# Performance work log

Measured on AMD Instinct MI355X. Metric: run time of the kernel, lower is better.

The kernel has to match this reference:

```python
import jax, jax.numpy as jnp
import numpy as np

DELTA_V = 0.5
DELTA_D = 1.5
ALPHA = 1.0
BETA = 1.0
GAMMA = 0.001
K = 33  # label ids 0..32; 0 = background (ignored)
EPS = 1e-12


def setup_inputs() -> dict:
    key = jax.random.key(0)
    k1, k2 = jax.random.split(key)
    B, N, E = 8, 65536, 32
    embeddings = jax.random.normal(k1, (B, N, E), dtype=jnp.float32)
    labels = jax.random.randint(k2, (B, N), 0, K)
    return {"embeddings": embeddings, "labels": labels}


def reference(embeddings, labels):
    B, N, E = embeddings.shape
    dt = embeddings.dtype
    seg = (labels + jnp.arange(B)[:, None] * K).reshape(-1)  # (B*N,)

    # segment mean -> per-instance centers (B, K, E)
    sums = jax.ops.segment_sum(embeddings.reshape(B * N, E), seg, num_segments=B * K).reshape(B, K, E)
    counts = jax.ops.segment_sum(jnp.ones((B * N,), dtype=dt), seg, num_segments=B * K).reshape(B, K)
    centers = sums / jnp.maximum(counts, 1.0)[..., None]

    present = counts > 0
    present = present.at[:, 0].set(False)  # drop background label 0
    presf = present.astype(dt)
    n_inst = presf.sum(axis=1)  # (B,)

    # ---- variance term: per-point hinge distance to own center, segment-mean ----
    c_per_point = centers[jnp.arange(B)[:, None], labels]  # (B, N, E) gather
    d2 = ((embeddings - c_per_point) ** 2).sum(-1)
    dist = jnp.sqrt(jnp.maximum(d2, EPS))
    hinge = jnp.where(labels > 0, jnp.maximum(dist - DELTA_V, 0.0), 0.0)
    per_inst_sum = jax.ops.segment_sum(hinge.reshape(-1), seg, num_segments=B * K).reshape(B, K)
    per_inst_mean = per_inst_sum / jnp.maximum(counts, 1.0)
    variance_term = (per_inst_mean * presf).sum(1) / jnp.maximum(n_inst, 1.0)

    # ---- distance term: pairwise hinge between present instance centers ----
    diff2 = ((centers[:, :, None, :] - centers[:, None, :, :]) ** 2).sum(-1)  # (B,K,K)
    upper = jnp.triu(jnp.ones((K, K), dtype=bool), 1)[None]
    pair_valid = present[:, :, None] & present[:, None, :] & upper
    cd = jnp.sqrt(jnp.maximum(jnp.where(pair_valid, diff2, 1.0), EPS))
    pair_hinge = jnp.maximum(2.0 * DELTA_D - cd, 0.0) * pair_valid.astype(dt)
    n_pairs = n_inst * (n_inst - 1.0) * 0.5
    distance_term = pair_hinge.sum((1, 2)) / jnp.maximum(n_pairs, 1.0)

    # ---- regularization: mean L2 norm of present centers ----
    c_norm = jnp.sqrt(jnp.maximum((centers ** 2).sum(-1), EPS))
    reg_term = (c_norm * presf).sum(1) / jnp.maximum(n_inst, 1.0)

    per_batch = ALPHA * variance_term + BETA * distance_term + GAMMA * reg_term
    per_batch = jnp.where(n_inst > 0, per_batch, 0.0)
    return per_batch.sum() / B
```

## Files before the change

### kernel.cpp

```cpp
#include <hip/hip_runtime.h>
#include <math.h>

#define KC 33
#define ED 32
#define KE (KC * ED)
#define PAD 33

#define BPB_A 64
#define TPA 128
#define NSLOT 8
#define BPB_H 128
#define TPH 256


__global__ void k_zero(float* __restrict__ ws, int n, float* __restrict__ out) {
    int i = blockIdx.x * blockDim.x + threadIdx.x;
    if (i < n) ws[i] = 0.f;
    if (i == 0) out[0] = 0.f;
}

__global__ __launch_bounds__(256) void k_accum(const float* __restrict__ emb,
                                               const int* __restrict__ lab,
                                               float* __restrict__ sums,
                                               float* __restrict__ counts, int N) {
    __shared__ float s_tile[TPA * PAD];
    __shared__ float s_priv[NSLOT * KE];
    __shared__ int   s_lab[TPA];
    __shared__ float s_hist[2 * KC];
    int t = threadIdx.x;
    for (int i = t; i < NSLOT * KE; i += 256) s_priv[i] = 0.f;
    if (t < 2 * KC) s_hist[t] = 0.f;

    int b     = blockIdx.x / BPB_A;
    int blk   = blockIdx.x % BPB_A;
    int chunk = N / BPB_A;
    int e     = t & 31;
    int slot  = t >> 5;
    size_t pbase = (size_t)b * N + (size_t)blk * chunk;
    const int NT = chunk / TPA;

    const float4* g4 = (const float4*)(emb + pbase * ED);
    float4 r0 = g4[t], r1 = g4[t + 256], r2 = g4[t + 512], r3 = g4[t + 768];
    int rl = 0;
    if (t < TPA) rl = lab[pbase + t];
    __syncthreads();

    for (int tb = 0; tb < NT; tb++) {
        {
            int f, p, m;
            f = t;        p = f >> 3; m = (f & 7) * 4;
            { float* d = &s_tile[PAD * p + m]; d[0]=r0.x; d[1]=r0.y; d[2]=r0.z; d[3]=r0.w; }
            f = t + 256;  p = f >> 3; m = (f & 7) * 4;
            { float* d = &s_tile[PAD * p + m]; d[0]=r1.x; d[1]=r1.y; d[2]=r1.z; d[3]=r1.w; }
            f = t + 512;  p = f >> 3; m = (f & 7) * 4;
            { float* d = &s_tile[PAD * p + m]; d[0]=r2.x; d[1]=r2.y; d[2]=r2.z; d[3]=r2.w; }
            f = t + 768;  p = f >> 3; m = (f & 7) * 4;
            { float* d = &s_tile[PAD * p + m]; d[0]=r3.x; d[1]=r3.y; d[2]=r3.z; d[3]=r3.w; }
        }
        if (t < TPA) {
            s_lab[t] = rl;
            atomicAdd(&s_hist[(t >> 6) * KC + rl], 1.f);
        }
        __syncthreads();

        if (tb + 1 < NT) {
            const float4* gn = (const float4*)(emb + (pbase + (size_t)(tb + 1) * TPA) * ED);
            r0 = gn[t]; r1 = gn[t + 256]; r2 = gn[t + 512]; r3 = gn[t + 768];
            if (t < TPA) rl = lab[pbase + (size_t)(tb + 1) * TPA + t];
        }

        float* priv = &s_priv[slot * KE];
#pragma unroll
        for (int st = 0; st < TPA / NSLOT; st++) {
            int pt = st * NSLOT + slot;
            float x = s_tile[pt * PAD + e];
            int   k = s_lab[pt];
            priv[k * ED + e] += x;
        }
        __syncthreads();
    }

    for (int i = t; i < KE; i += 256) {
        float v = 0.f;
#pragma unroll
        for (int s = 0; s < NSLOT; s++) v += s_priv[s * KE + i];
        atomicAdd(&sums[(size_t)b * KE + i], v);
    }
    if (t < KC)
        atomicAdd(&counts[b * KC + t], s_hist[t] + s_hist[KC + t]);
}

__global__ __launch_bounds__(256) void k_hinge(const float* __restrict__ emb,
                                               const int* __restrict__ lab,
                                               const float* __restrict__ sums,
                                               const float* __restrict__ counts,
                                               float* __restrict__ var, int N) {
    __shared__ float s_tile[TPH * PAD];
    __shared__ float s_ctr[KC * PAD];
    __shared__ float s_cnt[KC];
    __shared__ float s_inv[KC];
    __shared__ int   s_lab[TPH];
    __shared__ float s_red[4];
    int t     = threadIdx.x;
    int b     = blockIdx.x / BPB_H;
    int blk   = blockIdx.x % BPB_H;
    int chunk = N / BPB_H;
    size_t pbase = (size_t)b * N + (size_t)blk * chunk;
    const int NT = chunk / TPH;

    const float4* g4 = (const float4*)(emb + pbase * ED);
    float4 r0 = g4[t],        r1 = g4[t + 256],  r2 = g4[t + 512],  r3 = g4[t + 768];
    float4 r4 = g4[t + 1024], r5 = g4[t + 1280], r6 = g4[t + 1536], r7 = g4[t + 1792];
    int rl = lab[pbase + t];

    if (t < KC) {
        float c = counts[b * KC + t];
        s_cnt[t] = fmaxf(c, 1.f);
        s_inv[t] = (t > 0 && c > 0.f) ? 1.f / fmaxf(c, 1.f) : 0.f;
    }
    __syncthreads();
    for (int i = t; i < KE; i += 256) {
        int k = i >> 5, e = i & 31;
        s_ctr[k * PAD + e] = sums[(size_t)b * KE + i] / s_cnt[k];
    }

    float hs = 0.f;
    for (int tb = 0; tb < NT; tb++) {
        {
            int f, p, m;
            f = t;         p = f >> 3; m = (f & 7) * 4;
            { float* d = &s_tile[PAD * p + m]; d[0]=r0.x; d[1]=r0.y; d[2]=r0.z; d[3]=r0.w; }
            f = t + 256;   p = f >> 3; m = (f & 7) * 4;
            { float* d = &s_tile[PAD * p + m]; d[0]=r1.x; d[1]=r1.y; d[2]=r1.z; d[3]=r1.w; }
            f = t + 512;   p = f >> 3; m = (f & 7) * 4;
            { float* d = &s_tile[PAD * p + m]; d[0]=r2.x; d[1]=r2.y; d[2]=r2.z; d[3]=r2.w; }
            f = t + 768;   p = f >> 3; m = (f & 7) * 4;
            { float* d = &s_tile[PAD * p + m]; d[0]=r3.x; d[1]=r3.y; d[2]=r3.z; d[3]=r3.w; }
            f = t + 1024;  p = f >> 3; m = (f & 7) * 4;
            { float* d = &s_tile[PAD * p + m]; d[0]=r4.x; d[1]=r4.y; d[2]=r4.z; d[3]=r4.w; }
            f = t + 1280;  p = f >> 3; m = (f & 7) * 4;
            { float* d = &s_tile[PAD * p + m]; d[0]=r5.x; d[1]=r5.y; d[2]=r5.z; d[3]=r5.w; }
            f = t + 1536;  p = f >> 3; m = (f & 7) * 4;
            { float* d = &s_tile[PAD * p + m]; d[0]=r6.x; d[1]=r6.y; d[2]=r6.z; d[3]=r6.w; }
            f = t + 1792;  p = f >> 3; m = (f & 7) * 4;
            { float* d = &s_tile[PAD * p + m]; d[0]=r7.x; d[1]=r7.y; d[2]=r7.z; d[3]=r7.w; }
        }
        s_lab[t] = rl;
        __syncthreads();

        if (tb + 1 < NT) {
            const float4* gn = (const float4*)(emb + (pbase + (size_t)(tb + 1) * TPH) * ED);
            r0 = gn[t];        r1 = gn[t + 256];  r2 = gn[t + 512];  r3 = gn[t + 768];
            r4 = gn[t + 1024]; r5 = gn[t + 1280]; r6 = gn[t + 1536]; r7 = gn[t + 1792];
            rl = lab[pbase + (size_t)(tb + 1) * TPH + t];
        }

        int   k  = s_lab[t];
        float iv = s_inv[k];
        const float* xr = &s_tile[t * PAD];
        const float* cr = &s_ctr[k * PAD];
        float d2 = 0.f;
#pragma unroll
        for (int j = 0; j < ED; j++) {
            float d = xr[j] - cr[j];
            d2 = fmaf(d, d, d2);
        }
        float dist = sqrtf(fmaxf(d2, 1e-12f));
        hs += fmaxf(dist - 0.5f, 0.f) * iv;
        __syncthreads();
    }

    hs += __shfl_xor(hs, 1);  hs += __shfl_xor(hs, 2);  hs += __shfl_xor(hs, 4);
    hs += __shfl_xor(hs, 8);  hs += __shfl_xor(hs, 16); hs += __shfl_xor(hs, 32);
    if ((t & 63) == 0) s_red[t >> 6] = hs;
    __syncthreads();
    if (t == 0)
        atomicAdd(&var[b], s_red[0] + s_red[1] + s_red[2] + s_red[3]);
}

__global__ __launch_bounds__(256) void k_final(const float* __restrict__ sums,
                                               const float* __restrict__ counts,
                                               const float* __restrict__ var,
                                               float* __restrict__ out, int B) {
    __shared__ float s_ctr[KE];
    __shared__ float s_cnt[KC];
    __shared__ float s_reg[KC];
    __shared__ int   s_prs[KC];
    __shared__ float s_red[256];
    int b = blockIdx.x;
    int t = threadIdx.x;

    if (t < KC) {
        float c = counts[b * KC + t];
        s_cnt[t] = fmaxf(c, 1.f);
        s_prs[t] = (t > 0 && c > 0.f) ? 1 : 0;
    }
    __syncthreads();
    for (int i = t; i < KE; i += 256)
        s_ctr[i] = sums[(size_t)b * KE + i] / s_cnt[i >> 5];
    __syncthreads();
    if (t < KC) {
        float n2 = 0.f;
        for (int e2 = 0; e2 < ED; e2++) { float c = s_ctr[t * ED + e2]; n2 += c * c; }
        s_reg[t] = s_prs[t] ? sqrtf(fmaxf(n2, 1e-12f)) : 0.f;
    }
    __syncthreads();

    float psum = 0.f;
    for (int q = t; q < KC * KC; q += 256) {
        int i = q / KC, j = q % KC;
        if (i < j && s_prs[i] && s_prs[j]) {
            float d2 = 0.f;
            for (int e2 = 0; e2 < ED; e2++) {
                float d = s_ctr[i * ED + e2] - s_ctr[j * ED + e2];
                d2 += d * d;
            }
            float cd = sqrtf(fmaxf(d2, 1e-12f));
            psum += fmaxf(3.0f - cd, 0.f);
        }
    }
    s_red[t] = psum;
    __syncthreads();
    for (int s = 128; s > 0; s >>= 1) {
        if (t < s) s_red[t] += s_red[t + s];
        __syncthreads();
    }

    if (t == 0) {
        float reg = 0.f; int n = 0;
        for (int k = 0; k < KC; k++) { reg += s_reg[k]; n += s_prs[k]; }
        float nf = (float)n;
        float variance_term = var[b] / fmaxf(nf, 1.f);
        float npairs = nf * (nf - 1.f) * 0.5f;
        float distance_term = s_red[0] / fmaxf(npairs, 1.f);
        float reg_term = reg / fmaxf(nf, 1.f);
        float pb = variance_term + distance_term + 0.001f * reg_term;
        if (n == 0) pb = 0.f;
        atomicAdd(out, pb / (float)B);
    }
}

extern "C" void kernel_launch(void* const* d_in, const int* in_sizes, int n_in,
                              void* d_out, int out_size, void* d_ws, size_t ws_size,
                              hipStream_t stream) {
    const float* emb = (const float*)d_in[0];
    const int*   lab = (const int*)d_in[1];
    float* out = (float*)d_out;

    const int B = 8;
    const int N = in_sizes[1] / B;

    float* sums   = (float*)d_ws;
    float* counts = sums + (size_t)B * KE;
    float* var    = counts + (size_t)B * KC;

    int zn = B * KE + B * KC + B;
    k_zero<<<(zn + 255) / 256, 256, 0, stream>>>(sums, zn, out);
    k_accum<<<B * BPB_A, 256, 0, stream>>>(emb, lab, sums, counts, N);
    k_hinge<<<B * BPB_H, 256, 0, stream>>>(emb, lab, sums, counts, var, N);
    k_final<<<B, 256, 0, stream>>>(sums, counts, var, out, B);
}
```

Before: 131.0 us.

## Restructure hinge kernel to use 8-lane shuffle reduction instead of shared tile

The hinge kernel no longer stages embeddings through a padded shared-memory tile. Instead, eight lanes each own a float4 slice of a point, compute a partial squared distance against the center, and combine the partials with xor shuffles. Each block now covers one 256-point chunk, and the grid doubles the number of blocks per batch. This removes the shared-memory transpose and the per-tile barriers. The cost is shallower register prefetching (one float4 ahead instead of eight) and redundant sqrt/hinge work on the seven non-leader lanes.

```diff
diff --git a/kernel.cpp b/kernel.cpp
--- a/kernel.cpp
+++ b/kernel.cpp
@@ -9,8 +9,9 @@
 #define BPB_A 64
 #define TPA 128
 #define NSLOT 8
-#define BPB_H 128
-#define TPH 256
+#define BPB_H 256
+#define CPH 256
+#define NIT 8
 
 
 __global__ void k_zero(float* __restrict__ ws, int n, float* __restrict__ out) {
@@ -95,23 +96,19 @@
                                                const float* __restrict__ sums,
                                                const float* __restrict__ counts,
                                                float* __restrict__ var, int N) {
-    __shared__ float s_tile[TPH * PAD];
     __shared__ float s_ctr[KC * PAD];
     __shared__ float s_cnt[KC];
     __shared__ float s_inv[KC];
-    __shared__ int   s_lab[TPH];
+    __shared__ int   s_lab[CPH];
     __shared__ float s_red[4];
     int t     = threadIdx.x;
     int b     = blockIdx.x / BPB_H;
     int blk   = blockIdx.x % BPB_H;
-    int chunk = N / BPB_H;
-    size_t pbase = (size_t)b * N + (size_t)blk * chunk;
-    const int NT = chunk / TPH;
-
+    size_t pbase = (size_t)b * N + (size_t)blk * CPH;
     const float4* g4 = (const float4*)(emb + pbase * ED);
-    float4 r0 = g4[t],        r1 = g4[t + 256],  r2 = g4[t + 512],  r3 = g4[t + 768];
-    float4 r4 = g4[t + 1024], r5 = g4[t + 1280], r6 = g4[t + 1536], r7 = g4[t + 1792];
-    int rl = lab[pbase + t];
+
+    float4 xcur = g4[t];
+    s_lab[t] = lab[pbase + t];
 
     if (t < KC) {
         float c = counts[b * KC + t];
@@ -123,51 +120,29 @@
         int k = i >> 5, e = i & 31;
         s_ctr[k * PAD + e] = sums[(size_t)b * KE + i] / s_cnt[k];
     }
-
+    __syncthreads();
+
+    int q = t & 7;
     float hs = 0.f;
-    for (int tb = 0; tb < NT; tb++) {
-        {
-            int f, p, m;
-            f = t;         p = f >> 3; m = (f & 7) * 4;
-            { float* d = &s_tile[PAD * p + m]; d[0]=r0.x; d[1]=r0.y; d[2]=r0.z; d[3]=r0.w; }
-            f = t + 256;   p = f >> 3; m = (f & 7) * 4;
-            { float* d = &s_tile[PAD * p + m]; d[0]=r1.x; d[1]=r1.y; d[2]=r1.z; d[3]=r1.w; }
-            f = t + 512;   p = f >> 3; m = (f & 7) * 4;
-            { float* d = &s_tile[PAD * p + m]; d[0]=r2.x; d[1]=r2.y; d[2]=r2.z; d[3]=r2.w; }
-            f = t + 768;   p = f >> 3; m = (f & 7) * 4;
-            { float* d = &s_tile[PAD * p + m]; d[0]=r3.x; d[1]=r3.y; d[2]=r3.z; d[3]=r3.w; }
-            f = t + 1024;  p = f >> 3; m = (f & 7) * 4;
-            { float* d = &s_tile[PAD * p + m]; d[0]=r4.x; d[1]=r4.y; d[2]=r4.z; d[3]=r4.w; }
-            f = t + 1280;  p = f >> 3; m = (f & 7) * 4;
-            { float* d = &s_tile[PAD * p + m]; d[0]=r5.x; d[1]=r5.y; d[2]=r5.z; d[3]=r5.w; }
-            f = t + 1536;  p = f >> 3; m = (f & 7) * 4;
-            { float* d = &s_tile[PAD * p + m]; d[0]=r6.x; d[1]=r6.y; d[2]=r6.z; d[3]=r6.w; }
-            f = t + 1792;  p = f >> 3; m = (f & 7) * 4;
-            { float* d = &s_tile[PAD * p + m]; d[0]=r7.x; d[1]=r7.y; d[2]=r7.z; d[3]=r7.w; }
-        }
-        s_lab[t] = rl;
-        __syncthreads();
-
-        if (tb + 1 < NT) {
-            const float4* gn = (const float4*)(emb + (pbase + (size_t)(tb + 1) * TPH) * ED);
-            r0 = gn[t];        r1 = gn[t + 256];  r2 = gn[t + 512];  r3 = gn[t + 768];
-            r4 = gn[t + 1024]; r5 = gn[t + 1280]; r6 = gn[t + 1536]; r7 = gn[t + 1792];
-            rl = lab[pbase + (size_t)(tb + 1) * TPH + t];
-        }
-
-        int   k  = s_lab[t];
-        float iv = s_inv[k];
-        const float* xr = &s_tile[t * PAD];
-        const float* cr = &s_ctr[k * PAD];
-        float d2 = 0.f;
 #pragma unroll
-        for (int j = 0; j < ED; j++) {
-            float d = xr[j] - cr[j];
-            d2 = fmaf(d, d, d2);
-        }
+    for (int i = 0; i < NIT; i++) {
+        float4 xnext;
+        if (i + 1 < NIT) xnext = g4[(i + 1) * 256 + t];
+        int p_local = ((i << 8) + t) >> 3;
+        int k = s_lab[p_local];
+        const float* cr = &s_ctr[k * PAD + q * 4];
+        float d2 = 0.f, d;
+        d = xcur.x - cr[0]; d2 = fmaf(d, d, d2);
+        d = xcur.y - cr[1]; d2 = fmaf(d, d, d2);
+        d = xcur.z - cr[2]; d2 = fmaf(d, d, d2);
+        d = xcur.w - cr[3]; d2 = fmaf(d, d, d2);
+        d2 += __shfl_xor(d2, 1);
+        d2 += __shfl_xor(d2, 2);
+        d2 += __shfl_xor(d2, 4);
         float dist = sqrtf(fmaxf(d2, 1e-12f));
-        hs += fmaxf(dist - 0.5f, 0.f) * iv;
-        __syncthreads();
+        float hv = fmaxf(dist - 0.5f, 0.f) * s_inv[k];
+        hs += (q == 0) ? hv : 0.f;
+        xcur = xnext;
     }
 
     hs += __shfl_xor(hs, 1);  hs += __shfl_xor(hs, 2);  hs += __shfl_xor(hs, 4);
```

New measurement: 143.0 us. 1.09x slower.

## Use per-wave private staging to drop block barriers in accumulate and hinge kernels

Applied to the files above, without the earlier changes.

Both the accumulation and hinge kernels now stage embeddings in per-wavefront shared-memory strips instead of a block-wide tile. The main loops therefore need no __syncthreads, and only one barrier per kernel remains. The accumulation kernel doubles blocks per batch to 128, with each block handling 512 points in 16 small groups. Labels are loaded once up front as int2 and stored as 16-bit values. The intent is to remove barrier stalls and raise occupancy, at the cost of smaller per-iteration loads and less prefetch depth in the accumulation loop, plus more global atomics on the sums.

```diff
diff --git a/kernel.cpp b/kernel.cpp
--- a/kernel.cpp
+++ b/kernel.cpp
@@ -6,11 +6,8 @@
 #define KE (KC * ED)
 #define PAD 33
 
-#define BPB_A 64
-#define TPA 128
-#define NSLOT 8
+#define BPB_A 128
 #define BPB_H 128
-#define TPH 256
 
 
 __global__ void k_zero(float* __restrict__ ws, int n, float* __restrict__ out) {
@@ -23,67 +20,59 @@
                                                const int* __restrict__ lab,
                                                float* __restrict__ sums,
                                                float* __restrict__ counts, int N) {
-    __shared__ float s_tile[TPA * PAD];
-    __shared__ float s_priv[NSLOT * KE];
-    __shared__ int   s_lab[TPA];
+    __shared__ float s_stage[8 * 4 * PAD];
+    __shared__ float s_priv[8 * KE];
+    __shared__ unsigned short s_lab[512];
     __shared__ float s_hist[2 * KC];
     int t = threadIdx.x;
-    for (int i = t; i < NSLOT * KE; i += 256) s_priv[i] = 0.f;
-    if (t < 2 * KC) s_hist[t] = 0.f;
-
     int b     = blockIdx.x / BPB_A;
     int blk   = blockIdx.x % BPB_A;
     int chunk = N / BPB_A;
-    int e     = t & 31;
-    int slot  = t >> 5;
+    int e  = t & 31;
+    int s  = t >> 5;
+    int w  = t >> 6;
+    int h  = (t >> 5) & 1;
+    int l5 = t & 31;
     size_t pbase = (size_t)b * N + (size_t)blk * chunk;
-    const int NT = chunk / TPA;
-
     const float4* g4 = (const float4*)(emb + pbase * ED);
-    float4 r0 = g4[t], r1 = g4[t + 256], r2 = g4[t + 512], r3 = g4[t + 768];
-    int rl = 0;
-    if (t < TPA) rl = lab[pbase + t];
-    __syncthreads();
-
-    for (int tb = 0; tb < NT; tb++) {
+
+    for (int i = t; i < 8 * KE; i += 256) s_priv[i] = 0.f;
+    if (t < 2 * KC) s_hist[t] = 0.f;
+
+    int2 lp = ((const int2*)(lab + pbase))[t];
+    s_lab[2 * t]     = (unsigned short)lp.x;
+    s_lab[2 * t + 1] = (unsigned short)lp.y;
+    __syncthreads();
+    {
+        float* hh = &s_hist[(t >> 7) * KC];
+        atomicAdd(&hh[lp.x], 1.f);
+        atomicAdd(&hh[lp.y], 1.f);
+    }
+
+    float* strip = &s_stage[s * 4 * PAD];
+    float* priv  = &s_priv[s * KE];
+    int fbase = w * 1024 + h * 32 + l5;
+    float4 cur = g4[fbase];
+    for (int g = 0; g < 16; g++) {
         {
-            int f, p, m;
-            f = t;        p = f >> 3; m = (f & 7) * 4;
-            { float* d = &s_tile[PAD * p + m]; d[0]=r0.x; d[1]=r0.y; d[2]=r0.z; d[3]=r0.w; }
-            f = t + 256;  p = f >> 3; m = (f & 7) * 4;
-            { float* d = &s_tile[PAD * p + m]; d[0]=r1.x; d[1]=r1.y; d[2]=r1.z; d[3]=r1.w; }
-            f = t + 512;  p = f >> 3; m = (f & 7) * 4;
-            { float* d = &s_tile[PAD * p + m]; d[0]=r2.x; d[1]=r2.y; d[2]=r2.z; d[3]=r2.w; }
-            f = t + 768;  p = f >> 3; m = (f & 7) * 4;
-            { float* d = &s_tile[PAD * p + m]; d[0]=r3.x; d[1]=r3.y; d[2]=r3.z; d[3]=r3.w; }
-        }
-        if (t < TPA) {
-            s_lab[t] = rl;
-            atomicAdd(&s_hist[(t >> 6) * KC + rl], 1.f);
-        }
-        __syncthreads();
-
-        if (tb + 1 < NT) {
-            const float4* gn = (const float4*)(emb + (pbase + (size_t)(tb + 1) * TPA) * ED);
-            r0 = gn[t]; r1 = gn[t + 256]; r2 = gn[t + 512]; r3 = gn[t + 768];
-            if (t < TPA) rl = lab[pbase + (size_t)(tb + 1) * TPA + t];
-        }
-
-        float* priv = &s_priv[slot * KE];
+            float* d = &strip[(l5 >> 3) * PAD + (l5 & 7) * 4];
+            d[0] = cur.x; d[1] = cur.y; d[2] = cur.z; d[3] = cur.w;
+        }
+        if (g + 1 < 16) cur = g4[fbase + (g + 1) * 64];
+        int lbase = w * 128 + g * 8 + h * 4;
 #pragma unroll
-        for (int st = 0; st < TPA / NSLOT; st++) {
-            int pt = st * NSLOT + slot;
-            float x = s_tile[pt * PAD + e];
-            int   k = s_lab[pt];
+        for (int j = 0; j < 4; j++) {
+            float x = strip[j * PAD + e];
+            int   k = (int)s_lab[lbase + j];
             priv[k * ED + e] += x;
         }
-        __syncthreads();
-    }
+    }
+    __syncthreads();
 
     for (int i = t; i < KE; i += 256) {
         float v = 0.f;
 #pragma unroll
-        for (int s = 0; s < NSLOT; s++) v += s_priv[s * KE + i];
+        for (int c = 0; c < 8; c++) v += s_priv[c * KE + i];
         atomicAdd(&sums[(size_t)b * KE + i], v);
     }
     if (t < KC)
@@ -95,23 +84,23 @@
                                                const float* __restrict__ sums,
                                                const float* __restrict__ counts,
                                                float* __restrict__ var, int N) {
-    __shared__ float s_tile[TPH * PAD];
+    __shared__ float s_wtile[4 * 64 * PAD];
     __shared__ float s_ctr[KC * PAD];
     __shared__ float s_cnt[KC];
     __shared__ float s_inv[KC];
-    __shared__ int   s_lab[TPH];
+    __shared__ unsigned short s_lab[512];
     __shared__ float s_red[4];
-    int t     = threadIdx.x;
+    int t = threadIdx.x;
     int b     = blockIdx.x / BPB_H;
     int blk   = blockIdx.x % BPB_H;
     int chunk = N / BPB_H;
+    int w = t >> 6, l = t & 63;
     size_t pbase = (size_t)b * N + (size_t)blk * chunk;
-    const int NT = chunk / TPH;
-
     const float4* g4 = (const float4*)(emb + pbase * ED);
-    float4 r0 = g4[t],        r1 = g4[t + 256],  r2 = g4[t + 512],  r3 = g4[t + 768];
-    float4 r4 = g4[t + 1024], r5 = g4[t + 1280], r6 = g4[t + 1536], r7 = g4[t + 1792];
-    int rl = lab[pbase + t];
+
+    int2 lp = ((const int2*)(lab + pbase))[t];
+    s_lab[2 * t]     = (unsigned short)lp.x;
+    s_lab[2 * t + 1] = (unsigned short)lp.y;
 
     if (t < KC) {
         float c = counts[b * KC + t];
@@ -123,41 +112,43 @@
         int k = i >> 5, e = i & 31;
         s_ctr[k * PAD + e] = sums[(size_t)b * KE + i] / s_cnt[k];
     }
+    __syncthreads();
+
+    float* strip = &s_wtile[w * 64 * PAD];
+    int fb = w * 1024 + l;
+    float4 r0 = g4[fb],       r1 = g4[fb + 64],  r2 = g4[fb + 128], r3 = g4[fb + 192];
+    float4 r4 = g4[fb + 256], r5 = g4[fb + 320], r6 = g4[fb + 384], r7 = g4[fb + 448];
 
     float hs = 0.f;
-    for (int tb = 0; tb < NT; tb++) {
+    for (int g = 0; g < 2; g++) {
         {
             int f, p, m;
-            f = t;         p = f >> 3; m = (f & 7) * 4;
-            { float* d = &s_tile[PAD * p + m]; d[0]=r0.x; d[1]=r0.y; d[2]=r0.z; d[3]=r0.w; }
-            f = t + 256;   p = f >> 3; m = (f & 7) * 4;
-            { float* d = &s_tile[PAD * p + m]; d[0]=r1.x; d[1]=r1.y; d[2]=r1.z; d[3]=r1.w; }
-            f = t + 512;   p = f >> 3; m = (f & 7) * 4;
-            { float* d = &s_tile[PAD * p + m]; d[0]=r2.x; d[1]=r2.y; d[2]=r2.z; d[3]=r2.w; }
-            f = t + 768;   p = f >> 3; m = (f & 7) * 4;
-            { float* d = &s_tile[PAD * p + m]; d[0]=r3.x; d[1]=r3.y; d[2]=r3.z; d[3]=r3.w; }
-            f = t + 1024;  p = f >> 3; m = (f & 7) * 4;
-            { float* d = &s_tile[PAD * p + m]; d[0]=r4.x; d[1]=r4.y; d[2]=r4.z; d[3]=r4.w; }
-            f = t + 1280;  p = f >> 3; m = (f & 7) * 4;
-            { float* d = &s_tile[PAD * p + m]; d[0]=r5.x; d[1]=r5.y; d[2]=r5.z; d[3]=r5.w; }
-            f = t + 1536;  p = f >> 3; m = (f & 7) * 4;
-            { float* d = &s_tile[PAD * p + m]; d[0]=r6.x; d[1]=r6.y; d[2]=r6.z; d[3]=r6.w; }
-            f = t + 1792;  p = f >> 3; m = (f & 7) * 4;
-            { float* d = &s_tile[PAD * p + m]; d[0]=r7.x; d[1]=r7.y; d[2]=r7.z; d[3]=r7.w; }
-        }
-        s_lab[t] = rl;
-        __syncthreads();
-
-        if (tb + 1 < NT) {
-            const float4* gn = (const float4*)(emb + (pbase + (size_t)(tb + 1) * TPH) * ED);
-            r0 = gn[t];        r1 = gn[t + 256];  r2 = gn[t + 512];  r3 = gn[t + 768];
-            r4 = gn[t + 1024]; r5 = gn[t + 1280]; r6 = gn[t + 1536]; r7 = gn[t + 1792];
-            rl = lab[pbase + (size_t)(tb + 1) * TPH + t];
-        }
-
-        int   k  = s_lab[t];
+            f = l;        p = f >> 3; m = (f & 7) * 4;
+            { float* d = &strip[PAD * p + m]; d[0]=r0.x; d[1]=r0.y; d[2]=r0.z; d[3]=r0.w; }
+            f = l + 64;   p = f >> 3; m = (f & 7) * 4;
+            { float* d = &strip[PAD * p + m]; d[0]=r1.x; d[1]=r1.y; d[2]=r1.z; d[3]=r1.w; }
+            f = l + 128;  p = f >> 3; m = (f & 7) * 4;
+            { float* d = &strip[PAD * p + m]; d[0]=r2.x; d[1]=r2.y; d[2]=r2.z; d[3]=r2.w; }
+            f = l + 192;  p = f >> 3; m = (f & 7) * 4;
+            { float* d = &strip[PAD * p + m]; d[0]=r3.x; d[1]=r3.y; d[2]=r3.z; d[3]=r3.w; }
+            f = l + 256;  p = f >> 3; m = (f & 7) * 4;
+            { float* d = &strip[PAD * p + m]; d[0]=r4.x; d[1]=r4.y; d[2]=r4.z; d[3]=r4.w; }
+            f = l + 320;  p = f >> 3; m = (f & 7) * 4;
+            { float* d = &strip[PAD * p + m]; d[0]=r5.x; d[1]=r5.y; d[2]=r5.z; d[3]=r5.w; }
+            f = l + 384;  p = f >> 3; m = (f & 7) * 4;
+            { float* d = &strip[PAD * p + m]; d[0]=r6.x; d[1]=r6.y; d[2]=r6.z; d[3]=r6.w; }
+            f = l + 448;  p = f >> 3; m = (f & 7) * 4;
+            { float* d = &strip[PAD * p + m]; d[0]=r7.x; d[1]=r7.y; d[2]=r7.z; d[3]=r7.w; }
+        }
+        if (g + 1 < 2) {
+            int nb = fb + 512;
+            r0 = g4[nb];       r1 = g4[nb + 64];  r2 = g4[nb + 128]; r3 = g4[nb + 192];
+            r4 = g4[nb + 256]; r5 = g4[nb + 320]; r6 = g4[nb + 384]; r7 = g4[nb + 448];
+        }
+
+        int   k  = (int)s_lab[w * 128 + g * 64 + l];
         float iv = s_inv[k];
-        const float* xr = &s_tile[t * PAD];
+        const float* xr = &strip[l * PAD];
         const float* cr = &s_ctr[k * PAD];
         float d2 = 0.f;
 #pragma unroll
@@ -167,7 +158,6 @@
         }
         float dist = sqrtf(fmaxf(d2, 1e-12f));
         hs += fmaxf(dist - 0.5f, 0.f) * iv;
-        __syncthreads();
     }
 
     hs += __shfl_xor(hs, 1);  hs += __shfl_xor(hs, 2);  hs += __shfl_xor(hs, 4);
```

Result: faster. 127.8 us, median of 2 (-2.5%).
